# Kernel tuning notes

Measured on AMD Instinct MI355X. Metric: run time of the kernel, lower is better.

The kernel has to match this reference:

```python
import jax, jax.numpy as jnp
import numpy as np
from functools import partial

REG = 0.1
NUM_ITERS = 50
EPS_NORM = 1e-8
EPS_SINK = 1e-10


def _cdist(x0, x1):
    # torch.cdist(p=2): pairwise euclidean distance [B,N,N]
    sq0 = jnp.sum(x0 * x0, axis=-1)                     # [B,N]
    sq1 = jnp.sum(x1 * x1, axis=-1)                     # [B,N]
    inner = jnp.einsum('bnd,bmd->bnm', x0, x1)          # [B,N,N]
    d2 = sq0[:, :, None] + sq1[:, None, :] - 2.0 * inner
    return jnp.sqrt(jnp.maximum(d2, 0.0))


def setup_inputs() -> dict:
    key = jax.random.key(0)
    k0, k1 = jax.random.split(key)
    B, N, D = 8, 2048, 64
    x0 = jax.random.normal(k0, (B, N, D), dtype=jnp.float32)
    x1 = jax.random.normal(k1, (B, N, D), dtype=jnp.float32)
    return {"x0": x0, "x1": x1}


def reference(x0, x1):
    B, N, D = x0.shape
    # cost matrix + per-batch max normalization
    C = _cdist(x0, x1)
    C = C / (jnp.max(C, axis=(-2, -1), keepdims=True) + EPS_NORM)
    # Gibbs kernel
    K = jnp.exp(-C / REG)                               # [B,N,N]
    # Sinkhorn fixed-point iterations
    u0 = jnp.full((B, N), 1.0 / N, dtype=K.dtype)
    v0 = jnp.full((B, N), 1.0 / N, dtype=K.dtype)

    def body(i, uv):
        u, v = uv
        u = 1.0 / (jnp.einsum('bij,bj->bi', K, v) + EPS_SINK)
        v = 1.0 / (jnp.einsum('bij,bi->bj', K, u) + EPS_SINK)
        return (u, v)

    u, v = jax.lax.fori_loop(0, NUM_ITERS, body, (u0, v0))
    # transport plan P = diag(u) K diag(v)
    P = u[:, :, None] * K * v[:, None, :]               # [B,N,N]
    # greedy matching: argmax over columns
    matchings = jnp.argmax(P, axis=-1)                  # [B,N] int
    return matchings
```

## Files before the change

### kernel.cpp

```cpp
#include <hip/hip_runtime.h>
#include <hip/hip_bf16.h>
#include <stdint.h>

#define BB 8
#define NN 2048
#define DD 64
#define REGv 0.1f
#define NUM_ITERS 50
#define EPS_NORM 1e-8f
#define EPS_SINK 1e-10f
#define CHUNK 8
#define NBLK (NN / CHUNK)

__global__ void init_k(float* v, unsigned* maxd) {
    int t = blockIdx.x * 256 + threadIdx.x;
    if (t < BB * NN) v[t] = 1.0f / (float)NN;
    if (t < BB) maxd[t] = 0u;
}

__global__ void sq_k(const float* __restrict__ x0, const float* __restrict__ x1,
                     float* __restrict__ sq0, float* __restrict__ sq1) {
    int w = (blockIdx.x * 256 + threadIdx.x) >> 6;
    int lane = threadIdx.x & 63;
    if (w >= 2 * BB * NN) return;
    const float* src = (w < BB * NN) ? x0 : x1;
    int r = (w < BB * NN) ? w : w - BB * NN;
    float val = src[(size_t)r * DD + lane];
    float s = val * val;
    #pragma unroll
    for (int off = 32; off; off >>= 1) s += __shfl_xor(s, off);
    if (lane == 0) ((w < BB * NN) ? sq0 : sq1)[r] = s;
}

#define PAD 68
__global__ __launch_bounds__(256) void dist_k(const float* __restrict__ x0,
                                              const float* __restrict__ x1,
                                              const float* __restrict__ sq0,
                                              const float* __restrict__ sq1,
                                              float* __restrict__ Kd,
                                              unsigned* __restrict__ maxd) {
    __shared__ float x0s[64 * PAD];
    __shared__ float x1s[64 * PAD];
    __shared__ float wmax[4];
    int bid = blockIdx.x;
    int b = bid >> 10;
    int tile = bid & 1023;
    int ti = tile >> 5, tj = tile & 31;
    int i0 = ti * 64, j0 = tj * 64;
    int t = threadIdx.x;

    const float4* g0 = (const float4*)(x0 + ((size_t)b * NN + i0) * DD);
    const float4* g1 = (const float4*)(x1 + ((size_t)b * NN + j0) * DD);
    #pragma unroll
    for (int rep = 0; rep < 4; rep++) {
        int e = rep * 256 + t;
        int row = e >> 4, c4 = e & 15;
        float4 a = g0[row * 16 + c4];
        x0s[row * PAD + c4 * 4 + 0] = a.x; x0s[row * PAD + c4 * 4 + 1] = a.y;
        x0s[row * PAD + c4 * 4 + 2] = a.z; x0s[row * PAD + c4 * 4 + 3] = a.w;
        float4 c = g1[row * 16 + c4];
        x1s[row * PAD + c4 * 4 + 0] = c.x; x1s[row * PAD + c4 * 4 + 1] = c.y;
        x1s[row * PAD + c4 * 4 + 2] = c.z; x1s[row * PAD + c4 * 4 + 3] = c.w;
    }
    __syncthreads();

    int tx = t & 15, tyb = t >> 4;
    float acc[4][4];
    #pragma unroll
    for (int a = 0; a < 4; a++)
        #pragma unroll
        for (int c = 0; c < 4; c++) acc[a][c] = 0.0f;

    #pragma unroll
    for (int k4 = 0; k4 < 16; k4++) {
        float4 av[4], bv[4];
        #pragma unroll
        for (int di = 0; di < 4; di++)
            av[di] = *(const float4*)&x0s[(tyb * 4 + di) * PAD + k4 * 4];
        #pragma unroll
        for (int dj = 0; dj < 4; dj++)
            bv[dj] = *(const float4*)&x1s[(tx + 16 * dj) * PAD + k4 * 4];
        #pragma unroll
        for (int di = 0; di < 4; di++)
            #pragma unroll
            for (int dj = 0; dj < 4; dj++)
                acc[di][dj] += av[di].x * bv[dj].x + av[di].y * bv[dj].y +
                               av[di].z * bv[dj].z + av[di].w * bv[dj].w;
    }

    float lmax = 0.0f;
    #pragma unroll
    for (int di = 0; di < 4; di++) {
        float s0 = sq0[(size_t)b * NN + i0 + tyb * 4 + di];
        #pragma unroll
        for (int dj = 0; dj < 4; dj++) {
            float s1 = sq1[(size_t)b * NN + j0 + tx + 16 * dj];
            float d2 = s0 + s1 - 2.0f * acc[di][dj];
            float d = sqrtf(fmaxf(d2, 0.0f));
            lmax = fmaxf(lmax, d);
            Kd[((size_t)b * NN + i0 + tyb * 4 + di) * NN + j0 + tx + 16 * dj] = d;
        }
    }
    #pragma unroll
    for (int off = 32; off; off >>= 1) lmax = fmaxf(lmax, __shfl_xor(lmax, off));
    if ((t & 63) == 0) wmax[t >> 6] = lmax;
    __syncthreads();
    if (t == 0) {
        float m = fmaxf(fmaxf(wmax[0], wmax[1]), fmaxf(wmax[2], wmax[3]));
        atomicMax(&maxd[b], __float_as_uint(m));
    }
}

__global__ void expk_k(float* __restrict__ Kd, const unsigned* __restrict__ maxd) {
    size_t total4 = (size_t)BB * NN * NN / 4;
    for (size_t i4 = (size_t)blockIdx.x * 256 + threadIdx.x; i4 < total4;
         i4 += (size_t)gridDim.x * 256) {
        int b = (int)(i4 >> 20);
        float mv = __uint_as_float(maxd[b]) + EPS_NORM;
        float4 d4 = ((float4*)Kd)[i4];
        d4.x = expf(-((d4.x / mv) / REGv));
        d4.y = expf(-((d4.y / mv) / REGv));
        d4.z = expf(-((d4.z / mv) / REGv));
        d4.w = expf(-((d4.w / mv) / REGv));
        ((float4*)Kd)[i4] = d4;
    }
}

__global__ __launch_bounds__(256) void sink_k(const float* __restrict__ Kd,
                                              const float* __restrict__ v,
                                              float* __restrict__ u,
                                              float* __restrict__ partial) {
    __shared__ float red[4][CHUNK];
    int bid = blockIdx.x;
    int b = bid >> 8;
    int chunk = bid & 255;
    int row0 = chunk * CHUNK;
    int t = threadIdx.x;

    const float4* v4 = (const float4*)(v + (size_t)b * NN);
    float4 vA = v4[t], vB = v4[t + 256];

    const float4* Krow = (const float4*)(Kd + ((size_t)b * NN + row0) * NN);
    float4 kA[CHUNK], kB[CHUNK];
    #pragma unroll
    for (int r = 0; r < CHUNK; r++) {
        kA[r] = Krow[r * 512 + t];
        kB[r] = Krow[r * 512 + 256 + t];
    }

    float dp[CHUNK];
    #pragma unroll
    for (int r = 0; r < CHUNK; r++)
        dp[r] = kA[r].x * vA.x + kA[r].y * vA.y + kA[r].z * vA.z + kA[r].w * vA.w +
                kB[r].x * vB.x + kB[r].y * vB.y + kB[r].z * vB.z + kB[r].w * vB.w;
    #pragma unroll
    for (int r = 0; r < CHUNK; r++)
        #pragma unroll
        for (int off = 32; off; off >>= 1) dp[r] += __shfl_xor(dp[r], off);
    int lane = t & 63, w = t >> 6;
    if (lane == 0) {
        #pragma unroll
        for (int r = 0; r < CHUNK; r++) red[w][r] = dp[r];
    }
    __syncthreads();
    float uu[CHUNK];
    #pragma unroll
    for (int r = 0; r < CHUNK; r++)
        uu[r] = 1.0f / (red[0][r] + red[1][r] + red[2][r] + red[3][r] + EPS_SINK);
    if (t < CHUNK)
        u[(size_t)b * NN + row0 + t] =
            1.0f / (red[0][t] + red[1][t] + red[2][t] + red[3][t] + EPS_SINK);

    float4 accA = {0, 0, 0, 0}, accB = {0, 0, 0, 0};
    #pragma unroll
    for (int r = 0; r < CHUNK; r++) {
        accA.x += uu[r] * kA[r].x; accA.y += uu[r] * kA[r].y;
        accA.z += uu[r] * kA[r].z; accA.w += uu[r] * kA[r].w;
        accB.x += uu[r] * kB[r].x; accB.y += uu[r] * kB[r].y;
        accB.z += uu[r] * kB[r].z; accB.w += uu[r] * kB[r].w;
    }
    float4* p4 = (float4*)(partial + ((size_t)b * NBLK + chunk) * NN);
    p4[t] = accA;
    p4[t + 256] = accB;
}

__global__ void vred_k(const float* __restrict__ partial, float* __restrict__ v) {
    int j = blockIdx.x * 256 + threadIdx.x;
    int b = j >> 11, jj = j & 2047;
    const float* p = partial + (size_t)b * NBLK * NN + jj;
    float s = 0.0f;
    for (int c = 0; c < NBLK; c++) s += p[(size_t)c * NN];
    v[j] = 1.0f / (s + EPS_SINK);
}

__global__ __launch_bounds__(256) void argmax_k(const float* __restrict__ Kd,
                                                const float* __restrict__ u,
                                                const float* __restrict__ v,
                                                int* __restrict__ out) {
    int w = (blockIdx.x * 256 + threadIdx.x) >> 6;
    int lane = threadIdx.x & 63;
    int b = w >> 11, i = w & 2047;
    float uu = u[(size_t)b * NN + i];
    const float4* Kr = (const float4*)(Kd + ((size_t)b * NN + i) * NN);
    const float4* v4 = (const float4*)(v + (size_t)b * NN);
    float best = -1.0f;
    int bidx = 0;
    for (int it = 0; it < 8; it++) {
        int c4 = it * 64 + lane;
        float4 kk = Kr[c4];
        float4 vv = v4[c4];
        int j = c4 * 4;
        float p0 = (uu * kk.x) * vv.x;
        float p1 = (uu * kk.y) * vv.y;
        float p2 = (uu * kk.z) * vv.z;
        float p3 = (uu * kk.w) * vv.w;
        if (p0 > best) { best = p0; bidx = j; }
        if (p1 > best) { best = p1; bidx = j + 1; }
        if (p2 > best) { best = p2; bidx = j + 2; }
        if (p3 > best) { best = p3; bidx = j + 3; }
    }
    #pragma unroll
    for (int off = 32; off; off >>= 1) {
        float ov = __shfl_xor(best, off);
        int oi = __shfl_xor(bidx, off);
        if (ov > best || (ov == best && oi < bidx)) { best = ov; bidx = oi; }
    }
    if (lane == 0) out[(size_t)b * NN + i] = bidx;
}

extern "C" void kernel_launch(void* const* d_in, const int* in_sizes, int n_in,
                              void* d_out, int out_size, void* d_ws, size_t ws_size,
                              hipStream_t stream) {
    const float* x0 = (const float*)d_in[0];
    const float* x1 = (const float*)d_in[1];
    int* out = (int*)d_out;
    char* ws = (char*)d_ws;

    float* Kd      = (float*)(ws + 0ull);
    float* partial = (float*)(ws + 134217728ull);
    float* u       = (float*)(ws + 150994944ull);
    float* v       = (float*)(ws + 151060480ull);
    float* sq0     = (float*)(ws + 151126016ull);
    float* sq1     = (float*)(ws + 151191552ull);
    unsigned* maxd = (unsigned*)(ws + 151257088ull);

    init_k<<<64, 256, 0, stream>>>(v, maxd);
    sq_k<<<8192, 256, 0, stream>>>(x0, x1, sq0, sq1);
    dist_k<<<8192, 256, 0, stream>>>(x0, x1, sq0, sq1, Kd, maxd);
    expk_k<<<2048, 256, 0, stream>>>(Kd, maxd);
    for (int it = 0; it < NUM_ITERS; ++it) {
        sink_k<<<2048, 256, 0, stream>>>(Kd, v, u, partial);
        vred_k<<<64, 256, 0, stream>>>(partial, v);
    }
    argmax_k<<<4096, 256, 0, stream>>>(Kd, u, v, out);
}
```

Before: 1.951 ms.

## Recompute distances in two passes to fuse exp, enlarge Sinkhorn row chunks

The distance kernel now runs twice. The first pass only finds the per-batch maximum of squared distances, with no stores. The second pass recomputes the distances and writes exp(-C/reg) directly, which removes the write-then-read-modify-write round trip of the 128MB distance matrix through the separate exp kernel. The GEMM tile grows to 128x64 with a transposed x1 layout, and the Sinkhorn kernel uses 16-row chunks with 512 threads, which halves the partial-sum buffer that vred must reduce. The cost is recomputing the small 64-dim GEMM and holding more register state per thread.

```diff
diff --git a/kernel.cpp b/kernel.cpp
--- a/kernel.cpp
+++ b/kernel.cpp
@@ -9,7 +9,7 @@
 #define NUM_ITERS 50
 #define EPS_NORM 1e-8f
 #define EPS_SINK 1e-10f
-#define CHUNK 8
+#define CHUNK 16
 #define NBLK (NN / CHUNK)
 
 __global__ void init_k(float* v, unsigned* maxd) {
@@ -32,127 +32,122 @@
     if (lane == 0) ((w < BB * NN) ? sq0 : sq1)[r] = s;
 }
 
-#define PAD 68
-__global__ __launch_bounds__(256) void dist_k(const float* __restrict__ x0,
-                                              const float* __restrict__ x1,
-                                              const float* __restrict__ sq0,
-                                              const float* __restrict__ sq1,
-                                              float* __restrict__ Kd,
-                                              unsigned* __restrict__ maxd) {
-    __shared__ float x0s[64 * PAD];
-    __shared__ float x1s[64 * PAD];
-    __shared__ float wmax[4];
+template<int WRITE>
+__global__ __launch_bounds__(256) void distc_k(const float* __restrict__ x0,
+                                               const float* __restrict__ x1,
+                                               const float* __restrict__ sq0,
+                                               const float* __restrict__ sq1,
+                                               float* __restrict__ Kd,
+                                               unsigned* __restrict__ maxd) {
+    __shared__ float x0s[128 * 68];
+    __shared__ float x1t[64 * 68];
+    __shared__ float wred[4];
     int bid = blockIdx.x;
-    int b = bid >> 10;
-    int tile = bid & 1023;
+    int b = bid >> 9;
+    int tile = bid & 511;
     int ti = tile >> 5, tj = tile & 31;
-    int i0 = ti * 64, j0 = tj * 64;
+    int i0 = ti * 128, j0 = tj * 64;
     int t = threadIdx.x;
 
     const float4* g0 = (const float4*)(x0 + ((size_t)b * NN + i0) * DD);
+    #pragma unroll
+    for (int rep = 0; rep < 8; rep++) {
+        int e = rep * 256 + t;
+        int row = e >> 4, c4 = e & 15;
+        *(float4*)&x0s[row * 68 + c4 * 4] = g0[row * 16 + c4];
+    }
     const float4* g1 = (const float4*)(x1 + ((size_t)b * NN + j0) * DD);
     #pragma unroll
     for (int rep = 0; rep < 4; rep++) {
         int e = rep * 256 + t;
         int row = e >> 4, c4 = e & 15;
-        float4 a = g0[row * 16 + c4];
-        x0s[row * PAD + c4 * 4 + 0] = a.x; x0s[row * PAD + c4 * 4 + 1] = a.y;
-        x0s[row * PAD + c4 * 4 + 2] = a.z; x0s[row * PAD + c4 * 4 + 3] = a.w;
-        float4 c = g1[row * 16 + c4];
-        x1s[row * PAD + c4 * 4 + 0] = c.x; x1s[row * PAD + c4 * 4 + 1] = c.y;
-        x1s[row * PAD + c4 * 4 + 2] = c.z; x1s[row * PAD + c4 * 4 + 3] = c.w;
+        float4 a = g1[row * 16 + c4];
+        x1t[(c4 * 4 + 0) * 68 + row] = a.x;
+        x1t[(c4 * 4 + 1) * 68 + row] = a.y;
+        x1t[(c4 * 4 + 2) * 68 + row] = a.z;
+        x1t[(c4 * 4 + 3) * 68 + row] = a.w;
     }
     __syncthreads();
 
-    int tx = t & 15, tyb = t >> 4;
-    float acc[4][4];
-    #pragma unroll
-    for (int a = 0; a < 4; a++)
-        #pragma unroll
-        for (int c = 0; c < 4; c++) acc[a][c] = 0.0f;
+    int tx = t & 15, ty = t >> 4;
+    float4 acc4[8];
+    #pragma unroll
+    for (int di = 0; di < 8; di++) acc4[di] = make_float4(0.f, 0.f, 0.f, 0.f);
 
     #pragma unroll
     for (int k4 = 0; k4 < 16; k4++) {
-        float4 av[4], bv[4];
-        #pragma unroll
-        for (int di = 0; di < 4; di++)
-            av[di] = *(const float4*)&x0s[(tyb * 4 + di) * PAD + k4 * 4];
-        #pragma unroll
-        for (int dj = 0; dj < 4; dj++)
-            bv[dj] = *(const float4*)&x1s[(tx + 16 * dj) * PAD + k4 * 4];
-        #pragma unroll
-        for (int di = 0; di < 4; di++)
-            #pragma unroll
-            for (int dj = 0; dj < 4; dj++)
-                acc[di][dj] += av[di].x * bv[dj].x + av[di].y * bv[dj].y +
-                               av[di].z * bv[dj].z + av[di].w * bv[dj].w;
-    }
-
-    float lmax = 0.0f;
-    #pragma unroll
-    for (int di = 0; di < 4; di++) {
-        float s0 = sq0[(size_t)b * NN + i0 + tyb * 4 + di];
-        #pragma unroll
-        for (int dj = 0; dj < 4; dj++) {
-            float s1 = sq1[(size_t)b * NN + j0 + tx + 16 * dj];
-            float d2 = s0 + s1 - 2.0f * acc[di][dj];
-            float d = sqrtf(fmaxf(d2, 0.0f));
-            lmax = fmaxf(lmax, d);
-            Kd[((size_t)b * NN + i0 + tyb * 4 + di) * NN + j0 + tx + 16 * dj] = d;
-        }
-    }
-    #pragma unroll
-    for (int off = 32; off; off >>= 1) lmax = fmaxf(lmax, __shfl_xor(lmax, off));
-    if ((t & 63) == 0) wmax[t >> 6] = lmax;
-    __syncthreads();
-    if (t == 0) {
-        float m = fmaxf(fmaxf(wmax[0], wmax[1]), fmaxf(wmax[2], wmax[3]));
-        atomicMax(&maxd[b], __float_as_uint(m));
-    }
-}
-
-__global__ void expk_k(float* __restrict__ Kd, const unsigned* __restrict__ maxd) {
-    size_t total4 = (size_t)BB * NN * NN / 4;
-    for (size_t i4 = (size_t)blockIdx.x * 256 + threadIdx.x; i4 < total4;
-         i4 += (size_t)gridDim.x * 256) {
-        int b = (int)(i4 >> 20);
-        float mv = __uint_as_float(maxd[b]) + EPS_NORM;
-        float4 d4 = ((float4*)Kd)[i4];
-        d4.x = expf(-((d4.x / mv) / REGv));
-        d4.y = expf(-((d4.y / mv) / REGv));
-        d4.z = expf(-((d4.z / mv) / REGv));
-        d4.w = expf(-((d4.w / mv) / REGv));
-        ((float4*)Kd)[i4] = d4;
-    }
-}
-
-__global__ __launch_bounds__(256) void sink_k(const float* __restrict__ Kd,
+        float4 b0 = *(const float4*)&x1t[(k4 * 4 + 0) * 68 + tx * 4];
+        float4 b1 = *(const float4*)&x1t[(k4 * 4 + 1) * 68 + tx * 4];
+        float4 b2 = *(const float4*)&x1t[(k4 * 4 + 2) * 68 + tx * 4];
+        float4 b3 = *(const float4*)&x1t[(k4 * 4 + 3) * 68 + tx * 4];
+        #pragma unroll
+        for (int di = 0; di < 8; di++) {
+            float4 a = *(const float4*)&x0s[(ty * 8 + di) * 68 + k4 * 4];
+            acc4[di].x += a.x * b0.x + a.y * b1.x + a.z * b2.x + a.w * b3.x;
+            acc4[di].y += a.x * b0.y + a.y * b1.y + a.z * b2.y + a.w * b3.y;
+            acc4[di].z += a.x * b0.z + a.y * b1.z + a.z * b2.z + a.w * b3.z;
+            acc4[di].w += a.x * b0.w + a.y * b1.w + a.z * b2.w + a.w * b3.w;
+        }
+    }
+
+    int ib = b * NN + i0 + ty * 8;
+    float4 s1 = *(const float4*)&sq1[b * NN + j0 + tx * 4];
+
+    if (WRITE) {
+        float mv = sqrtf(__uint_as_float(maxd[b])) + EPS_NORM;
+        #pragma unroll
+        for (int di = 0; di < 8; di++) {
+            float s0 = sq0[ib + di];
+            float4 o;
+            o.x = expf(-((sqrtf(fmaxf(s0 + s1.x - 2.f * acc4[di].x, 0.f)) / mv) / REGv));
+            o.y = expf(-((sqrtf(fmaxf(s0 + s1.y - 2.f * acc4[di].y, 0.f)) / mv) / REGv));
+            o.z = expf(-((sqrtf(fmaxf(s0 + s1.z - 2.f * acc4[di].z, 0.f)) / mv) / REGv));
+            o.w = expf(-((sqrtf(fmaxf(s0 + s1.w - 2.f * acc4[di].w, 0.f)) / mv) / REGv));
+            *(float4*)&Kd[(size_t)(ib + di) * NN + j0 + tx * 4] = o;
+        }
+    } else {
+        float lm = 0.0f;
+        #pragma unroll
+        for (int di = 0; di < 8; di++) {
+            float s0 = sq0[ib + di];
+            lm = fmaxf(lm, fmaxf(s0 + s1.x - 2.f * acc4[di].x, 0.f));
+            lm = fmaxf(lm, fmaxf(s0 + s1.y - 2.f * acc4[di].y, 0.f));
+            lm = fmaxf(lm, fmaxf(s0 + s1.z - 2.f * acc4[di].z, 0.f));
+            lm = fmaxf(lm, fmaxf(s0 + s1.w - 2.f * acc4[di].w, 0.f));
+        }
+        #pragma unroll
+        for (int off = 32; off; off >>= 1) lm = fmaxf(lm, __shfl_xor(lm, off));
+        if ((t & 63) == 0) wred[t >> 6] = lm;
+        __syncthreads();
+        if (t == 0) {
+            float m = fmaxf(fmaxf(wred[0], wred[1]), fmaxf(wred[2], wred[3]));
+            atomicMax(&maxd[b], __float_as_uint(m));
+        }
+    }
+}
+
+__global__ __launch_bounds__(512) void sink_k(const float* __restrict__ Kd,
                                               const float* __restrict__ v,
                                               float* __restrict__ u,
                                               float* __restrict__ partial) {
-    __shared__ float red[4][CHUNK];
+    __shared__ float red[8][CHUNK];
+    __shared__ float uu_s[CHUNK];
     int bid = blockIdx.x;
-    int b = bid >> 8;
-    int chunk = bid & 255;
+    int b = bid >> 7;
+    int chunk = bid & 127;
     int row0 = chunk * CHUNK;
     int t = threadIdx.x;
 
-    const float4* v4 = (const float4*)(v + (size_t)b * NN);
-    float4 vA = v4[t], vB = v4[t + 256];
-
-    const float4* Krow = (const float4*)(Kd + ((size_t)b * NN + row0) * NN);
-    float4 kA[CHUNK], kB[CHUNK];
-    #pragma unroll
-    for (int r = 0; r < CHUNK; r++) {
-        kA[r] = Krow[r * 512 + t];
-        kB[r] = Krow[r * 512 + 256 + t];
-    }
+    float4 vv = ((const float4*)(v + (size_t)b * NN))[t];
+    const float4* Kr = (const float4*)(Kd + ((size_t)b * NN + row0) * NN);
+    float4 kk[CHUNK];
+    #pragma unroll
+    for (int r = 0; r < CHUNK; r++) kk[r] = Kr[r * 512 + t];
 
     float dp[CHUNK];
     #pragma unroll
     for (int r = 0; r < CHUNK; r++)
-        dp[r] = kA[r].x * vA.x + kA[r].y * vA.y + kA[r].z * vA.z + kA[r].w * vA.w +
-                kB[r].x * vB.x + kB[r].y * vB.y + kB[r].z * vB.z + kB[r].w * vB.w;
+        dp[r] = kk[r].x * vv.x + kk[r].y * vv.y + kk[r].z * vv.z + kk[r].w * vv.w;
     #pragma unroll
     for (int r = 0; r < CHUNK; r++)
         #pragma unroll
@@ -163,25 +158,24 @@
         for (int r = 0; r < CHUNK; r++) red[w][r] = dp[r];
     }
     __syncthreads();
-    float uu[CHUNK];
-    #pragma unroll
-    for (int r = 0; r < CHUNK; r++)
-        uu[r] = 1.0f / (red[0][r] + red[1][r] + red[2][r] + red[3][r] + EPS_SINK);
-    if (t < CHUNK)
-        u[(size_t)b * NN + row0 + t] =
-            1.0f / (red[0][t] + red[1][t] + red[2][t] + red[3][t] + EPS_SINK);
-
-    float4 accA = {0, 0, 0, 0}, accB = {0, 0, 0, 0};
+    if (t < CHUNK) {
+        float s = 0.0f;
+        #pragma unroll
+        for (int c = 0; c < 8; c++) s += red[c][t];
+        float uu = 1.0f / (s + EPS_SINK);
+        uu_s[t] = uu;
+        u[(size_t)b * NN + row0 + t] = uu;
+    }
+    __syncthreads();
+
+    float4 acc = make_float4(0.f, 0.f, 0.f, 0.f);
     #pragma unroll
     for (int r = 0; r < CHUNK; r++) {
-        accA.x += uu[r] * kA[r].x; accA.y += uu[r] * kA[r].y;
-        accA.z += uu[r] * kA[r].z; accA.w += uu[r] * kA[r].w;
-        accB.x += uu[r] * kB[r].x; accB.y += uu[r] * kB[r].y;
-        accB.z += uu[r] * kB[r].z; accB.w += uu[r] * kB[r].w;
-    }
-    float4* p4 = (float4*)(partial + ((size_t)b * NBLK + chunk) * NN);
-    p4[t] = accA;
-    p4[t + 256] = accB;
+        float uur = uu_s[r];
+        acc.x += uur * kk[r].x; acc.y += uur * kk[r].y;
+        acc.z += uur * kk[r].z; acc.w += uur * kk[r].w;
+    }
+    ((float4*)(partial + ((size_t)b * NBLK + chunk) * NN))[t] = acc;
 }
 
 __global__ void vred_k(const float* __restrict__ partial, float* __restrict__ v) {
@@ -238,18 +232,18 @@
 
     float* Kd      = (float*)(ws + 0ull);
     float* partial = (float*)(ws + 134217728ull);
-    float* u       = (float*)(ws + 150994944ull);
-    float* v       = (float*)(ws + 151060480ull);
-    float* sq0     = (float*)(ws + 151126016ull);
-    float* sq1     = (float*)(ws + 151191552ull);
-    unsigned* maxd = (unsigned*)(ws + 151257088ull);
+    float* u       = (float*)(ws + 142606336ull);
+    float* v       = (float*)(ws + 142671872ull);
+    float* sq0     = (float*)(ws + 142737408ull);
+    float* sq1     = (float*)(ws + 142802944ull);
+    unsigned* maxd = (unsigned*)(ws + 142868480ull);
 
     init_k<<<64, 256, 0, stream>>>(v, maxd);
     sq_k<<<8192, 256, 0, stream>>>(x0, x1, sq0, sq1);
-    dist_k<<<8192, 256, 0, stream>>>(x0, x1, sq0, sq1, Kd, maxd);
-    expk_k<<<2048, 256, 0, stream>>>(Kd, maxd);
+    distc_k<0><<<4096, 256, 0, stream>>>(x0, x1, sq0, sq1, Kd, maxd);
+    distc_k<1><<<4096, 256, 0, stream>>>(x0, x1, sq0, sq1, Kd, maxd);
     for (int it = 0; it < NUM_ITERS; ++it) {
-        sink_k<<<2048, 256, 0, stream>>>(Kd, v, u, partial);
+        sink_k<<<1024, 512, 0, stream>>>(Kd, v, u, partial);
         vred_k<<<64, 256, 0, stream>>>(partial, v);
     }
     argmax_k<<<4096, 256, 0, stream>>>(Kd, u, v, out);
```

Result: faster. 1.661 ms (-14.9%).
